# Kernel tuning notes

Measured on AMD Instinct MI355X. Metric: run time of the kernel, lower is better.

Reference implementation:

```python
import jax, jax.numpy as jnp
import numpy as np

N = 512      # N_res
C = 128      # act_dim == num_intermediate_channel
EPS = 1e-5   # torch LayerNorm default


def _layernorm(x, w, b):
    mu = jnp.mean(x, axis=-1, keepdims=True)
    var = jnp.var(x, axis=-1, keepdims=True)
    return (x - mu) * jax.lax.rsqrt(var + EPS) * w + b


def setup_inputs() -> dict:
    key = jax.random.key(0)
    ks = jax.random.split(key, 12)
    s_in = 1.0 / np.sqrt(C)
    inp = {
        "act": jax.random.normal(ks[0], (N, N, C), dtype=jnp.float32),
        "mask": jax.random.uniform(ks[1], (N, N), dtype=jnp.float32),
        # left_norm_input (LayerNorm over act_dim)
        "ln_in_w": jnp.ones((C,), jnp.float32),
        "ln_in_b": jnp.zeros((C,), jnp.float32),
        # projection: Linear(C -> 2C)
        "proj_w": jax.random.uniform(ks[2], (2 * C, C), jnp.float32, -s_in, s_in),
        "proj_b": jax.random.uniform(ks[3], (2 * C,), jnp.float32, -s_in, s_in),
        # gate: Linear(C -> 2C)
        "gate_w": jax.random.uniform(ks[4], (2 * C, C), jnp.float32, -s_in, s_in),
        "gate_b": jax.random.uniform(ks[5], (2 * C,), jnp.float32, -s_in, s_in),
        # center_norm (LayerNorm over num_intermediate_channel)
        "cn_w": jnp.ones((C,), jnp.float32),
        "cn_b": jnp.zeros((C,), jnp.float32),
        # output_projection: Linear(C -> C)
        "outp_w": jax.random.uniform(ks[6], (C, C), jnp.float32, -s_in, s_in),
        "outp_b": jax.random.uniform(ks[7], (C,), jnp.float32, -s_in, s_in),
        # gating_linear: Linear(C -> C)
        "gl_w": jax.random.uniform(ks[8], (C, C), jnp.float32, -s_in, s_in),
        "gl_b": jax.random.uniform(ks[9], (C,), jnp.float32, -s_in, s_in),
    }
    return inp


def reference(act, mask, ln_in_w, ln_in_b, proj_w, proj_b, gate_w, gate_b,
              cn_w, cn_b, outp_w, outp_b, gl_w, gl_b):
    m = mask[..., None]                                  # [N,N,1]
    x = _layernorm(act, ln_in_w, ln_in_b)                # [N,N,C]
    input_act = x
    proj = m * (jnp.einsum('ijc,dc->ijd', x, proj_w) + proj_b)      # [N,N,2C]
    proj = proj * jax.nn.sigmoid(jnp.einsum('ijc,dc->ijd', x, gate_w) + gate_b)
    left, right = proj[..., :C], proj[..., C:]           # each [N,N,C]
    # outgoing-edges triangular multiplication
    out = jnp.einsum('ikc,jkc->ijc', left, right)        # [N,N,C]
    out = _layernorm(out, cn_w, cn_b)
    out = jnp.einsum('ijc,dc->ijd', out, outp_w) + outp_b
    out = out * jax.nn.sigmoid(jnp.einsum('ijc,dc->ijd', input_act, gl_w) + gl_b)
    return out
```

## Files before the change

### kernel.cpp

```cpp
#include <hip/hip_runtime.h>
#include <hip/hip_bf16.h>


constexpr int TN = 512;
constexpr int TC = 128;
constexpr int TNP = TN * TN;
constexpr float TEPS = 1e-5f;

typedef __attribute__((ext_vector_type(8))) short s8b;
typedef __attribute__((ext_vector_type(4))) float f4;

__device__ __forceinline__ float wredsum(float v) {
#pragma unroll
    for (int off = 32; off > 0; off >>= 1) v += __shfl_xor(v, off);
    return v;
}
__device__ __forceinline__ float sigmoidf(float x) { return 1.0f / (1.0f + __expf(-x)); }
__device__ __forceinline__ unsigned short bfbits(float f) {
    __hip_bfloat16 h = __float2bfloat16(f);
    return *reinterpret_cast<unsigned short*>(&h);
}
__device__ __forceinline__ float bf2f(unsigned short u) {
    return __uint_as_float(((unsigned int)u) << 16);
}


extern "C" __global__ __launch_bounds__(256)
void k_wconv(const float* __restrict__ pw, const float* __restrict__ gw,
             const float* __restrict__ ow, const float* __restrict__ glw,
             __hip_bfloat16* __restrict__ warr, __hip_bfloat16* __restrict__ wcat2)
{
    const int idx = blockIdx.x * 256 + threadIdx.x;
    if (idx < 65536) {
        const int j = idx & 7;
        const int slot = (idx >> 3) & 63;
        const int kg = (idx >> 9) & 3;
        const int rg = (idx >> 11) & 7;
        const int nc = idx >> 14;
        const int lh = slot & 15, lq = slot >> 4;
        const int row = rg * 16 + lh;
        const int k = kg * 32 + lq * 8 + j;
        const float v = (row < 64) ? pw[(nc * 64 + row) * TC + k]
                                   : gw[(nc * 64 + (row - 64)) * TC + k];
        warr[idx] = __float2bfloat16(v);
    } else if (idx < 98304) {
        const int j = idx - 65536;
        wcat2[j] = __float2bfloat16(j < 16384 ? ow[j] : glw[j - 16384]);
    }
}

extern "C" __global__ __launch_bounds__(256)
void k_ln(const float* __restrict__ act, const float* __restrict__ lnw,
          const float* __restrict__ lnb, __hip_bfloat16* __restrict__ xhp)
{
    __shared__ __align__(16) unsigned short t16[16 * 136];
    const int t = threadIdx.x, lane = t & 63, w = t >> 6;
    const int P0 = blockIdx.x * 64;
    const float2 wv = ((const float2*)lnw)[lane];
    const float2 bv = ((const float2*)lnb)[lane];
    unsigned short* xb = (unsigned short*)xhp;

    for (int r = 0; r < 4; ++r) {
#pragma unroll
        for (int q = 0; q < 4; ++q) {
            const int prow = w * 4 + q;
            const int p = P0 + r * 16 + prow;
            const float2 a = ((const float2*)(act + (size_t)p * TC))[lane];
            const float mu = wredsum(a.x + a.y) * (1.0f / 128.0f);
            const float d0 = a.x - mu, d1 = a.y - mu;
            const float var = wredsum(d0 * d0 + d1 * d1) * (1.0f / 128.0f);
            const float rs = rsqrtf(var + TEPS);
            ushort2 o;
            o.x = bfbits(d0 * rs * wv.x + bv.x);
            o.y = bfbits(d1 * rs * wv.y + bv.y);
            *(ushort2*)&t16[prow * 136 + lane * 2] = o;
        }
        __syncthreads();
        {
            const int kg = t >> 6, lq = (t >> 4) & 3, lh = t & 15;
            const s8b v = *(const s8b*)&t16[lh * 136 + kg * 32 + lq * 8];
            *(s8b*)(xb + (size_t)((P0 >> 4) + r) * 2048 + (size_t)t * 8) = v;
        }
        __syncthreads();
    }
}

extern "C" __global__ __launch_bounds__(256)
void k_proj(const __hip_bfloat16* __restrict__ xhp, const float* __restrict__ mask,
            const __hip_bfloat16* __restrict__ warr,
            const float* __restrict__ proj_b, const float* __restrict__ gate_b,
            __hip_bfloat16* __restrict__ lt, __hip_bfloat16* __restrict__ rt)
{
    __shared__ __align__(16) unsigned short Xls[128 * TC];
    __shared__ __align__(16) unsigned short Wls[128 * TC];
    __shared__ float msk[128];
    unsigned short* tls = Xls;

    const int t = threadIdx.x, lane = t & 63, w = t >> 6;
    const int lh = lane & 15, lq = lane >> 4;

    const int bid = blockIdx.x;
    const int work = (bid & 7) * 1024 + (bid >> 3);
    const int pt = work >> 2, dt = work & 3;
    const int P0 = pt * 128;

    const unsigned short* xb = (const unsigned short*)xhp;
    const unsigned short* wb = (const unsigned short*)warr;

    if (t < 128) msk[t] = mask[P0 + t];

#pragma unroll
    for (int s = 0; s < 8; ++s) {
        const int u = w * 8 + s;
        const size_t gu = ((size_t)(P0 >> 4) + (u >> 2)) * 4 + (u & 3);
        __builtin_amdgcn_global_load_lds(
            (const __attribute__((address_space(1))) unsigned*)(xb + gu * 512 + (size_t)lane * 8),
            (__attribute__((address_space(3))) unsigned*)&Xls[u * 512], 16, 0, 0);
    }
#pragma unroll
    for (int s = 0; s < 8; ++s) {
        const int u = w * 8 + s;
        __builtin_amdgcn_global_load_lds(
            (const __attribute__((address_space(1))) unsigned*)(wb + ((size_t)dt * 32 + u) * 512 + (size_t)lane * 8),
            (__attribute__((address_space(3))) unsigned*)&Wls[u * 512], 16, 0, 0);
    }
    __syncthreads();

    const int wm = w >> 1, wn = w & 1;

    f4 acc[4][4];
#pragma unroll
    for (int mi = 0; mi < 4; ++mi)
#pragma unroll
        for (int ni = 0; ni < 4; ++ni)
            acc[mi][ni] = (f4){0.f, 0.f, 0.f, 0.f};

#pragma unroll
    for (int kg = 0; kg < 4; ++kg) {
        s8b af[4], bfr[4];
#pragma unroll
        for (int mi = 0; mi < 4; ++mi)
            af[mi] = *(const s8b*)&Xls[(((wm * 4 + mi) * 4) + kg) * 512 + lane * 8];
#pragma unroll
        for (int nd = 0; nd < 2; ++nd) {
            bfr[nd]     = *(const s8b*)&Wls[(((wn * 2 + nd) * 4) + kg) * 512 + lane * 8];
            bfr[2 + nd] = *(const s8b*)&Wls[((((4 + wn * 2 + nd)) * 4) + kg) * 512 + lane * 8];
        }
#pragma unroll
        for (int mi = 0; mi < 4; ++mi)
#pragma unroll
            for (int ni = 0; ni < 4; ++ni)
                acc[mi][ni] = __builtin_amdgcn_mfma_f32_16x16x32_bf16(
                    af[mi], bfr[ni], acc[mi][ni], 0, 0, 0);
    }
    __syncthreads();

#pragma unroll
    for (int mi = 0; mi < 4; ++mi)
#pragma unroll
        for (int nd = 0; nd < 2; ++nd) {
            const int dl = wn * 32 + nd * 16 + lh;
            const float pbv = proj_b[dt * 64 + dl];
            const float gbv = gate_b[dt * 64 + dl];
            const f4 P = acc[mi][nd];
            const f4 G = acc[mi][2 + nd];
            const int pbase = wm * 64 + mi * 16 + lq * 4;
            float v[4];
#pragma unroll
            for (int r = 0; r < 4; ++r)
                v[r] = msk[pbase + r] * (P[r] + pbv) * sigmoidf(G[r] + gbv);
            ushort2 u01, u23;
            u01.x = bfbits(v[0]); u01.y = bfbits(v[1]);
            u23.x = bfbits(v[2]); u23.y = bfbits(v[3]);
            *(ushort2*)&tls[dl * 134 + pbase]     = u01;
            *(ushort2*)&tls[dl * 134 + pbase + 2] = u23;
        }
    __syncthreads();

    {
        __hip_bfloat16* dst0 = (dt < 2) ? lt + (size_t)(dt * 64) * TNP
                                        : rt + (size_t)((dt - 2) * 64) * TNP;
#pragma unroll
        for (int rr = 0; rr < 16; ++rr) {
            const int dl = w * 16 + rr;
            const ushort2 v = *(const ushort2*)&tls[dl * 134 + lane * 2];
            *(ushort2*)((unsigned short*)(dst0 + (size_t)dl * TNP) + P0 + lane * 2) = v;
        }
    }
}

extern "C" __global__ __launch_bounds__(256)
void k_tri_mfma(const __hip_bfloat16* __restrict__ lt,
                const __hip_bfloat16* __restrict__ rt,
                __hip_bfloat16* __restrict__ trih)
{
    __shared__ __align__(16) char smem[128 * 136 * 2];
    __hip_bfloat16* Als = (__hip_bfloat16*)smem;
    __hip_bfloat16* Bls = (__hip_bfloat16*)(smem + 8192);
    unsigned short* Cls = (unsigned short*)smem;

    const int bid = blockIdx.x;
    const int work = (bid & 7) * 256 + (bid >> 3);
    const int c = work >> 4, tt = work & 15;
    const int i0 = (tt >> 2) * 128, j0 = (tt & 3) * 128;

    const int t = threadIdx.x;
    const int w = t >> 6, lane = t & 63;
    const int wm = w >> 1, wn = w & 1;
    const int lh = lane & 15, lq = lane >> 4;

    const size_t cbase = (size_t)c * TNP;
    const int srow = lane >> 2;
    const int scol = (lane & 3) * 8;

    f4 acc[4][4];
#pragma unroll
    for (int mi = 0; mi < 4; ++mi)
#pragma unroll
        for (int ni = 0; ni < 4; ++ni)
            acc[mi][ni] = (f4){0.f, 0.f, 0.f, 0.f};

    for (int k0 = 0; k0 < TN; k0 += 32) {
        __syncthreads();
#pragma unroll
        for (int s = 0; s < 2; ++s) {
            const int r0 = w * 32 + s * 16;
            const __hip_bfloat16* ga = lt + cbase + (size_t)(i0 + r0 + srow) * TN + k0 + scol;
            const __hip_bfloat16* gb = rt + cbase + (size_t)(j0 + r0 + srow) * TN + k0 + scol;
            __builtin_amdgcn_global_load_lds(
                (const __attribute__((address_space(1))) unsigned*)ga,
                (__attribute__((address_space(3))) unsigned*)&Als[r0 * 32], 16, 0, 0);
            __builtin_amdgcn_global_load_lds(
                (const __attribute__((address_space(1))) unsigned*)gb,
                (__attribute__((address_space(3))) unsigned*)&Bls[r0 * 32], 16, 0, 0);
        }
        __syncthreads();

        s8b afr[4], bfr[4];
#pragma unroll
        for (int mi = 0; mi < 4; ++mi)
            afr[mi] = *(const s8b*)&Als[(wm * 64 + mi * 16 + lh) * 32 + lq * 8];
#pragma unroll
        for (int ni = 0; ni < 4; ++ni)
            bfr[ni] = *(const s8b*)&Bls[(wn * 64 + ni * 16 + lh) * 32 + lq * 8];
#pragma unroll
        for (int mi = 0; mi < 4; ++mi)
#pragma unroll
            for (int ni = 0; ni < 4; ++ni)
                acc[mi][ni] = __builtin_amdgcn_mfma_f32_16x16x32_bf16(
                    afr[mi], bfr[ni], acc[mi][ni], 0, 0, 0);
    }

    __syncthreads();
#pragma unroll
    for (int mi = 0; mi < 4; ++mi)
#pragma unroll
        for (int ni = 0; ni < 4; ++ni) {
            const f4 v = acc[mi][ni];
            const int jl = wn * 64 + ni * 16 + lh;
#pragma unroll
            for (int r = 0; r < 4; ++r) {
                const int il = wm * 64 + mi * 16 + lq * 4 + r;
                Cls[il * 136 + jl] = bfbits(v[r]);
            }
        }
    __syncthreads();
    {
        unsigned short* ob = (unsigned short*)trih + cbase;
#pragma unroll
        for (int qq = 0; qq < 8; ++qq) {
            const int row = qq * 16 + (t >> 4);
            const int c16 = t & 15;
            const s8b v = *(const s8b*)&Cls[row * 136 + c16 * 8];
            *(s8b*)&ob[(size_t)(i0 + row) * TN + j0 + c16 * 8] = v;
        }
    }
}

constexpr int PB = 64;

extern "C" __global__ __launch_bounds__(256)
void k_out_proj(const __hip_bfloat16* __restrict__ trih,
                const __hip_bfloat16* __restrict__ xhp,
                const float* __restrict__ cnw, const float* __restrict__ cnb,
                const __hip_bfloat16* __restrict__ wcat2,
                const float* __restrict__ outp_b, const float* __restrict__ gl_b,
                float* __restrict__ outb)
{
    __shared__ unsigned short ysb[PB * 134];
    __shared__ __align__(16) unsigned short Yls[PB * TC];

    const int t = threadIdx.x, lane = t & 63, w = t >> 6;
    const int lh = lane & 15, lq = lane >> 4;
    const int P0 = blockIdx.x * PB;
    const unsigned short* tb = (const unsigned short*)trih;
    const unsigned short* xb = (const unsigned short*)xhp;
    const unsigned short* wb = (const unsigned short*)wcat2;

    {
        const int c0 = t >> 5, pp = (t & 31) * 2;
#pragma unroll
        for (int cc = 0; cc < 16; ++cc) {
            const int ch = cc * 8 + c0;
            const ushort2 v = *(const ushort2*)(tb + (size_t)ch * TNP + P0 + pp);
            ysb[pp * 134 + ch] = v.x;
            ysb[(pp + 1) * 134 + ch] = v.y;
        }
    }
    __syncthreads();

    {
        const float2 wv = ((const float2*)cnw)[lane];
        const float2 bv = ((const float2*)cnb)[lane];
        const int sw = (lane >> 2) & 7;
#pragma unroll 2
        for (int it = 0; it < 16; ++it) {
            const int pl = it * 4 + w;
            const ushort2 uv = *(const ushort2*)&ysb[pl * 134 + lane * 2];
            const float a0 = bf2f(uv.x), a1 = bf2f(uv.y);
            const float mu = wredsum(a0 + a1) * (1.0f / 128.0f);
            const float d0 = a0 - mu, d1 = a1 - mu;
            const float var = wredsum(d0 * d0 + d1 * d1) * (1.0f / 128.0f);
            const float rs = rsqrtf(var + TEPS);
            ushort2 o;
            o.x = bfbits(d0 * rs * wv.x + bv.x);
            o.y = bfbits(d1 * rs * wv.y + bv.y);
            const int chunk = ((pl >> 4) * 4 + (lane >> 4)) * 64
                            + ((lane >> 2) & 3) * 16 + ((pl & 15) ^ sw);
            *(ushort2*)&Yls[chunk * 8 + (lane & 3) * 2] = o;
        }
    }
    __syncthreads();

    const int dO = w * 32;
    const int dG = 128 + w * 32;

    f4 acc[4][4];
#pragma unroll
    for (int mi = 0; mi < 4; ++mi)
#pragma unroll
        for (int ni = 0; ni < 4; ++ni)
            acc[mi][ni] = (f4){0.f, 0.f, 0.f, 0.f};

#pragma unroll
    for (int kg = 0; kg < 4; ++kg) {
        s8b bo[2], bg[2], ay[4], ah[4];
#pragma unroll
        for (int nd = 0; nd < 2; ++nd) {
            bo[nd] = *(const s8b*)(wb + (dO + nd * 16 + lh) * TC + kg * 32 + lq * 8);
            bg[nd] = *(const s8b*)(wb + (dG + nd * 16 + lh) * TC + kg * 32 + lq * 8);
        }
        const int rsw = (kg * 4 + lq) & 7;
#pragma unroll
        for (int mi = 0; mi < 4; ++mi) {
            const int chunk = (mi * 4 + kg) * 64 + lq * 16 + (lh ^ rsw);
            ay[mi] = *(const s8b*)&Yls[chunk * 8];
            ah[mi] = *(const s8b*)(xb + (size_t)((P0 >> 4) + mi) * 2048
                                      + kg * 512 + (size_t)lane * 8);
        }
#pragma unroll
        for (int mi = 0; mi < 4; ++mi)
#pragma unroll
            for (int nd = 0; nd < 2; ++nd) {
                acc[mi][nd]     = __builtin_amdgcn_mfma_f32_16x16x32_bf16(
                    ay[mi], bo[nd], acc[mi][nd], 0, 0, 0);
                acc[mi][2 + nd] = __builtin_amdgcn_mfma_f32_16x16x32_bf16(
                    ah[mi], bg[nd], acc[mi][2 + nd], 0, 0, 0);
            }
    }

    float ob[2], gb2[2];
#pragma unroll
    for (int nd = 0; nd < 2; ++nd) {
        ob[nd]  = outp_b[w * 32 + nd * 16 + lh];
        gb2[nd] = gl_b[w * 32 + nd * 16 + lh];
    }
#pragma unroll
    for (int mi = 0; mi < 4; ++mi)
#pragma unroll
        for (int nd = 0; nd < 2; ++nd) {
            const f4 O = acc[mi][nd];
            const f4 G = acc[mi][2 + nd];
            const int d = w * 32 + nd * 16 + lh;
#pragma unroll
            for (int r = 0; r < 4; ++r) {
                const int p = P0 + mi * 16 + lq * 4 + r;
                outb[(size_t)p * TC + d] = (O[r] + ob[nd]) * sigmoidf(G[r] + gb2[nd]);
            }
        }
}

extern "C" void kernel_launch(void* const* d_in, const int* in_sizes, int n_in,
                              void* d_out, int out_size, void* d_ws, size_t ws_size,
                              hipStream_t stream)
{
    const float* act    = (const float*)d_in[0];
    const float* mask   = (const float*)d_in[1];
    const float* lnw    = (const float*)d_in[2];
    const float* lnb    = (const float*)d_in[3];
    const float* proj_w = (const float*)d_in[4];
    const float* proj_b = (const float*)d_in[5];
    const float* gate_w = (const float*)d_in[6];
    const float* gate_b = (const float*)d_in[7];
    const float* cnw    = (const float*)d_in[8];
    const float* cnb    = (const float*)d_in[9];
    const float* outp_w = (const float*)d_in[10];
    const float* outp_b = (const float*)d_in[11];
    const float* gl_w   = (const float*)d_in[12];
    const float* gl_b   = (const float*)d_in[13];

    __hip_bfloat16* lt   = (__hip_bfloat16*)d_ws;
    __hip_bfloat16* rt   = lt + (size_t)TC * TNP;
    __hip_bfloat16* xhp  = rt + (size_t)TC * TNP;
    __hip_bfloat16* trih = xhp + (size_t)TNP * TC;
    __hip_bfloat16* warr = trih + (size_t)TC * TNP;
    __hip_bfloat16* wcat2 = warr + 4 * 128 * TC;
    float* out = (float*)d_out;

    k_wconv<<<384, 256, 0, stream>>>(proj_w, gate_w, outp_w, gl_w, warr, wcat2);
    k_ln<<<TNP / 64, 256, 0, stream>>>(act, lnw, lnb, xhp);
    k_proj<<<8192, 256, 0, stream>>>(xhp, mask, warr, proj_b, gate_b, lt, rt);
    k_tri_mfma<<<2048, 256, 0, stream>>>(lt, rt, trih);
    k_out_proj<<<TNP / PB, 256, 0, stream>>>(trih, xhp, cnw, cnb, wcat2,
                                             outp_b, gl_b, out);
}
```

Baseline: 298.3 us.

## Fold center LayerNorm into output projection via per-row mean/rstd correction

The center LayerNorm weight is folded into the output projection weights, and two per-channel vectors (S = W·cnw, T = W·cnb + bias) are precomputed by a new tiny kernel. The out-projection kernel now feeds the raw bf16 triangle output to the MFMA directly. Per-row mean and rstd come from a block reduction and are applied afterwards as o = rstd*acc - rstd*mu*S + T. This drops the normalize-and-rewrite pass and the second LDS tile, but uses the one-pass E[x^2]-mu^2 variance and runs the GEMM on unnormalized bf16 values, which may cost accuracy.

```diff
diff --git a/kernel.cpp b/kernel.cpp
--- a/kernel.cpp
+++ b/kernel.cpp
@@ -28,6 +28,7 @@
 extern "C" __global__ __launch_bounds__(256)
 void k_wconv(const float* __restrict__ pw, const float* __restrict__ gw,
              const float* __restrict__ ow, const float* __restrict__ glw,
+             const float* __restrict__ cnw,
              __hip_bfloat16* __restrict__ warr, __hip_bfloat16* __restrict__ wcat2)
 {
     const int idx = blockIdx.x * 256 + threadIdx.x;
@@ -45,8 +46,29 @@
         warr[idx] = __float2bfloat16(v);
     } else if (idx < 98304) {
         const int j = idx - 65536;
-        wcat2[j] = __float2bfloat16(j < 16384 ? ow[j] : glw[j - 16384]);
-    }
+        if (j < 16384) {
+            const int c = j & 127;
+            wcat2[j] = __float2bfloat16(cnw[c] * ow[j]);
+        } else {
+            wcat2[j] = __float2bfloat16(glw[j - 16384]);
+        }
+    }
+}
+
+extern "C" __global__ __launch_bounds__(128)
+void k_sdt(const float* __restrict__ ow, const float* __restrict__ cnw,
+           const float* __restrict__ cnb, const float* __restrict__ outp_b,
+           float* __restrict__ Svec, float* __restrict__ Tbvec)
+{
+    const int d = threadIdx.x;
+    float S = 0.f, T = 0.f;
+    for (int c = 0; c < TC; ++c) {
+        const float w = ow[d * TC + c];
+        S += cnw[c] * w;
+        T += cnb[c] * w;
+    }
+    Svec[d] = S;
+    Tbvec[d] = T + outp_b[d];
 }
 
 extern "C" __global__ __launch_bounds__(256)
@@ -282,13 +304,14 @@
 extern "C" __global__ __launch_bounds__(256)
 void k_out_proj(const __hip_bfloat16* __restrict__ trih,
                 const __hip_bfloat16* __restrict__ xhp,
-                const float* __restrict__ cnw, const float* __restrict__ cnb,
                 const __hip_bfloat16* __restrict__ wcat2,
-                const float* __restrict__ outp_b, const float* __restrict__ gl_b,
+                const float* __restrict__ Svec, const float* __restrict__ Tbvec,
+                const float* __restrict__ gl_b,
                 float* __restrict__ outb)
 {
-    __shared__ unsigned short ysb[PB * 134];
-    __shared__ __align__(16) unsigned short Yls[PB * TC];
+    __shared__ __align__(16) unsigned short ysb[PB * 136];
+    __shared__ float2 sred[4][PB];
+    __shared__ float2 stats[PB];
 
     const int t = threadIdx.x, lane = t & 63, w = t >> 6;
     const int lh = lane & 15, lq = lane >> 4;
@@ -303,32 +326,37 @@
         for (int cc = 0; cc < 16; ++cc) {
             const int ch = cc * 8 + c0;
             const ushort2 v = *(const ushort2*)(tb + (size_t)ch * TNP + P0 + pp);
-            ysb[pp * 134 + ch] = v.x;
-            ysb[(pp + 1) * 134 + ch] = v.y;
+            ysb[pp * 136 + ch] = v.x;
+            ysb[(pp + 1) * 136 + ch] = v.y;
         }
     }
     __syncthreads();
 
     {
-        const float2 wv = ((const float2*)cnw)[lane];
-        const float2 bv = ((const float2*)cnb)[lane];
-        const int sw = (lane >> 2) & 7;
-#pragma unroll 2
-        for (int it = 0; it < 16; ++it) {
-            const int pl = it * 4 + w;
-            const ushort2 uv = *(const ushort2*)&ysb[pl * 134 + lane * 2];
-            const float a0 = bf2f(uv.x), a1 = bf2f(uv.y);
-            const float mu = wredsum(a0 + a1) * (1.0f / 128.0f);
-            const float d0 = a0 - mu, d1 = a1 - mu;
-            const float var = wredsum(d0 * d0 + d1 * d1) * (1.0f / 128.0f);
-            const float rs = rsqrtf(var + TEPS);
-            ushort2 o;
-            o.x = bfbits(d0 * rs * wv.x + bv.x);
-            o.y = bfbits(d1 * rs * wv.y + bv.y);
-            const int chunk = ((pl >> 4) * 4 + (lane >> 4)) * 64
-                            + ((lane >> 2) & 3) * 16 + ((pl & 15) ^ sw);
-            *(ushort2*)&Yls[chunk * 8 + (lane & 3) * 2] = o;
-        }
+        const int pl = lane;
+        float s = 0.f, s2 = 0.f;
+#pragma unroll
+        for (int kk = 0; kk < 4; ++kk) {
+            const s8b v = *(const s8b*)&ysb[pl * 136 + w * 32 + kk * 8];
+#pragma unroll
+            for (int j = 0; j < 8; ++j) {
+                const float f = bf2f((unsigned short)v[j]);
+                s += f; s2 += f * f;
+            }
+        }
+        sred[w][pl] = make_float2(s, s2);
+    }
+    __syncthreads();
+    if (t < PB) {
+        float s = 0.f, s2 = 0.f;
+#pragma unroll
+        for (int g = 0; g < 4; ++g) {
+            const float2 v = sred[g][t];
+            s += v.x; s2 += v.y;
+        }
+        const float mu = s * (1.0f / 128.0f);
+        const float var = s2 * (1.0f / 128.0f) - mu * mu;
+        stats[t] = make_float2(mu, rsqrtf(var + TEPS));
     }
     __syncthreads();
 
@@ -350,11 +378,9 @@
             bo[nd] = *(const s8b*)(wb + (dO + nd * 16 + lh) * TC + kg * 32 + lq * 8);
             bg[nd] = *(const s8b*)(wb + (dG + nd * 16 + lh) * TC + kg * 32 + lq * 8);
         }
-        const int rsw = (kg * 4 + lq) & 7;
 #pragma unroll
         for (int mi = 0; mi < 4; ++mi) {
-            const int chunk = (mi * 4 + kg) * 64 + lq * 16 + (lh ^ rsw);
-            ay[mi] = *(const s8b*)&Yls[chunk * 8];
+            ay[mi] = *(const s8b*)&ysb[(mi * 16 + lh) * 136 + kg * 32 + lq * 8];
             ah[mi] = *(const s8b*)(xb + (size_t)((P0 >> 4) + mi) * 2048
                                       + kg * 512 + (size_t)lane * 8);
         }
@@ -369,23 +395,27 @@
             }
     }
 
-    float ob[2], gb2[2];
+    float Sd[2], Tbd[2], glb[2];
 #pragma unroll
     for (int nd = 0; nd < 2; ++nd) {
-        ob[nd]  = outp_b[w * 32 + nd * 16 + lh];
-        gb2[nd] = gl_b[w * 32 + nd * 16 + lh];
+        const int d = w * 32 + nd * 16 + lh;
+        Sd[nd]  = Svec[d];
+        Tbd[nd] = Tbvec[d];
+        glb[nd] = gl_b[d];
     }
 #pragma unroll
     for (int mi = 0; mi < 4; ++mi)
 #pragma unroll
         for (int nd = 0; nd < 2; ++nd) {
-            const f4 O = acc[mi][nd];
-            const f4 G = acc[mi][2 + nd];
+            const f4 G = acc[mi][nd];
+            const f4 Gg = acc[mi][2 + nd];
             const int d = w * 32 + nd * 16 + lh;
 #pragma unroll
             for (int r = 0; r < 4; ++r) {
-                const int p = P0 + mi * 16 + lq * 4 + r;
-                outb[(size_t)p * TC + d] = (O[r] + ob[nd]) * sigmoidf(G[r] + gb2[nd]);
+                const int ploc = mi * 16 + lq * 4 + r;
+                const float2 st = stats[ploc];
+                const float o = st.y * G[r] - st.y * st.x * Sd[nd] + Tbd[nd];
+                outb[(size_t)(P0 + ploc) * TC + d] = o * sigmoidf(Gg[r] + glb[nd]);
             }
         }
 }
@@ -415,12 +445,15 @@
     __hip_bfloat16* trih = xhp + (size_t)TNP * TC;
     __hip_bfloat16* warr = trih + (size_t)TC * TNP;
     __hip_bfloat16* wcat2 = warr + 4 * 128 * TC;
+    float* Svec  = (float*)(wcat2 + 2 * TC * TC);
+    float* Tbvec = Svec + TC;
     float* out = (float*)d_out;
 
-    k_wconv<<<384, 256, 0, stream>>>(proj_w, gate_w, outp_w, gl_w, warr, wcat2);
+    k_wconv<<<384, 256, 0, stream>>>(proj_w, gate_w, outp_w, gl_w, cnw, warr, wcat2);
+    k_sdt<<<1, 128, 0, stream>>>(outp_w, cnw, cnb, outp_b, Svec, Tbvec);
     k_ln<<<TNP / 64, 256, 0, stream>>>(act, lnw, lnb, xhp);
     k_proj<<<8192, 256, 0, stream>>>(xhp, mask, warr, proj_b, gate_b, lt, rt);
     k_tri_mfma<<<2048, 256, 0, stream>>>(lt, rt, trih);
-    k_out_proj<<<TNP / PB, 256, 0, stream>>>(trih, xhp, cnw, cnb, wcat2,
-                                             outp_b, gl_b, out);
-}
+    k_out_proj<<<TNP / PB, 256, 0, stream>>>(trih, xhp, wcat2, Svec, Tbvec,
+                                             gl_b, out);
+}
```

Result: no change. 294.8 us (-1.2%).
